# Optimization experiments

Hardware: AMD Instinct MI355X
Metric: run time of the kernel (lower is better)

The kernel has to match this reference:

```python
import jax, jax.numpy as jnp
import numpy as np

MIN_NORM = 1e-15
BALL_EPS = 4e-3  # hgcn PoincareBall eps for float32
C = 1.0          # c_in = c_out = 1


def _artanh(x):
    return jnp.arctanh(jnp.clip(x, -1.0 + 1e-7, 1.0 - 1e-7))


def _norm(x):
    return jnp.clip(jnp.linalg.norm(x, axis=-1, keepdims=True), MIN_NORM)


def proj(x, c=C):
    n = _norm(x)
    maxnorm = (1.0 - BALL_EPS) / jnp.sqrt(c)
    return jnp.where(n > maxnorm, x / n * maxnorm, x)


def expmap0(u, c=C):
    sc = jnp.sqrt(c)
    n = _norm(u)
    return jnp.tanh(sc * n) * u / (sc * n)


def logmap0(p, c=C):
    sc = jnp.sqrt(c)
    n = _norm(p)
    return _artanh(sc * n) * p / (sc * n)


def mobius_add(x, y, c=C):
    x2 = jnp.sum(x * x, -1, keepdims=True)
    y2 = jnp.sum(y * y, -1, keepdims=True)
    xy = jnp.sum(x * y, -1, keepdims=True)
    num = (1 + 2 * c * xy + c * y2) * x + (1 - c * x2) * y
    den = 1 + 2 * c * xy + c * c * x2 * y2
    return num / jnp.clip(den, MIN_NORM)


def mobius_matvec(m, x, c=C):
    # m: [out, in] torch-Linear layout; mx = x @ m.T
    sc = jnp.sqrt(c)
    xn = _norm(x)
    mx = x @ m.T
    mxn = _norm(mx)
    res = jnp.tanh(mxn / xn * _artanh(sc * xn)) * mx / (mxn * sc)
    zero = jnp.all(mx == 0, axis=-1, keepdims=True)
    return jnp.where(zero, jnp.zeros_like(res), res)


def hyp_linear(x, w, b, c=C):
    res = proj(mobius_matvec(w, x, c), c)
    hyp_bias = proj(expmap0(b[None, :], c), c)  # proj_tan0 is identity on Poincare ball
    return proj(mobius_add(res, hyp_bias, c), c)


def hyp_act(x, c_in=C, c_out=C):
    xt = jax.nn.relu(logmap0(x, c_in))
    return proj(expmap0(xt, c_out), c_out)


def mean_agg(h, src, dst, n):
    # mean of source-node features over incoming edges per destination node
    s = jax.ops.segment_sum(h[src], dst, num_segments=n)
    deg = jax.ops.segment_sum(jnp.ones((src.shape[0],), h.dtype), dst, num_segments=n)
    return s / jnp.clip(deg, 1.0)[:, None]


def setup_inputs() -> dict:
    key = jax.random.key(0)
    N, D, E = 100000, 128, 1600000  # in_features = out_features = 128
    ks = jax.random.split(key, 20)
    inp = {
        "x": jax.random.normal(ks[0], (N, D), jnp.float32) * 0.01,  # keep near ball origin
        "src_pos": jax.random.randint(ks[1], (E,), 0, N, jnp.int32),
        "dst_pos": jax.random.randint(ks[2], (E,), 0, N, jnp.int32),
        "src_neg": jax.random.randint(ks[3], (E,), 0, N, jnp.int32),
        "dst_neg": jax.random.randint(ks[4], (E,), 0, N, jnp.int32),
    }
    s = 0.01
    inp["W1b"] = jax.random.normal(ks[5], (D, 2 * D), jnp.float32) * s
    inp["b1b"] = jax.random.normal(ks[6], (D,), jnp.float32) * s
    inp["W1h"] = jax.random.normal(ks[7], (D, 2 * D), jnp.float32) * s
    inp["b1h"] = jax.random.normal(ks[8], (D,), jnp.float32) * s
    inp["W2b"] = jax.random.normal(ks[9], (2 * D, 3 * D), jnp.float32) * s
    inp["b2b"] = jax.random.normal(ks[10], (2 * D,), jnp.float32) * s
    inp["W2h"] = jax.random.normal(ks[11], (2 * D, 3 * D), jnp.float32) * s
    inp["b2h"] = jax.random.normal(ks[12], (2 * D,), jnp.float32) * s
    inp["W3b"] = jax.random.normal(ks[13], (D, 2 * D), jnp.float32) * s
    inp["b3b"] = jax.random.normal(ks[14], (D,), jnp.float32) * s
    inp["W3h"] = jax.random.normal(ks[15], (D, 2 * D), jnp.float32) * s
    inp["b3h"] = jax.random.normal(ks[16], (D,), jnp.float32) * s
    return inp


def reference(x, src_pos, dst_pos, src_neg, dst_neg,
              W1b, b1b, W1h, b1h, W2b, b2b, W2h, b2h, W3b, b3b, W3h, b3h):
    n = x.shape[0]
    # layer-1 signed neighbor means over x
    pos1 = mean_agg(x, src_pos, dst_pos, n)
    neg1 = mean_agg(x, src_neg, dst_neg, n)
    h_b1 = hyp_act(hyp_linear(jnp.concatenate([pos1, x], axis=1), W1b, b1b))
    h_n1 = hyp_act(hyp_linear(jnp.concatenate([neg1, x], axis=1), W1h, b1h))
    # layer-2 balance-theory aggregation over (h_b1, h_n1)
    pos2 = jnp.concatenate([mean_agg(h_b1, src_pos, dst_pos, n),
                            mean_agg(h_n1, src_neg, dst_neg, n)], axis=1)
    neg2 = jnp.concatenate([mean_agg(h_n1, src_pos, dst_pos, n),
                            mean_agg(h_b1, src_neg, dst_neg, n)], axis=1)
    h_b2 = hyp_act(hyp_linear(jnp.concatenate([pos2, h_b1], axis=1), W2b, b2b))
    h_n2 = hyp_act(hyp_linear(jnp.concatenate([neg2, h_n1], axis=1), W2h, b2h))
    h_b3 = hyp_act(hyp_linear(h_b2, W3b, b3b))
    h_n3 = hyp_act(hyp_linear(h_n2, W3h, b3h))
    return jnp.concatenate([h_b3, h_n3, x], axis=1)  # [N, 3*D]
```

## Files before the change

kernel.cpp:

```cpp
#include <hip/hip_runtime.h>
#include <cstdint>
#include <cstddef>

#define DEV __device__ __forceinline__

typedef unsigned int uint32;
typedef unsigned short ushort16;
typedef __bf16 bfx8 __attribute__((ext_vector_type(8)));
typedef float f32x4 __attribute__((ext_vector_type(4)));

constexpr int D = 128;
constexpr int CAP = 64;
constexpr float MINN  = 1e-15f;
constexpr float MAXN  = 1.0f - 4e-3f;
constexpr float ACLIP = 1.0f - 1e-7f;

DEV float wave_sum(float v) {
#pragma unroll
  for (int off = 32; off > 0; off >>= 1) v += __shfl_xor(v, off, 64);
  return v;
}

DEV float artanh_clip(float x) {
  x = fminf(x, ACLIP);
  return 0.5f * logf((1.0f + x) / (1.0f - x));
}

DEV uint32 f2b(float f) {
  uint32 u = __float_as_uint(f);
  u += 0x7fffu + ((u >> 16) & 1u);
  return u >> 16;
}
DEV float b2f_lo(uint32 v) { return __uint_as_float(v << 16); }
DEV float b2f_hi(uint32 v) { return __uint_as_float(v & 0xffff0000u); }

__global__ void zero_k(int* p, int n) {
  int i = blockIdx.x * 256 + threadIdx.x;
  if (i < n) p[i] = 0;
}

__global__ __launch_bounds__(256) void fillc_k(
    const int* __restrict__ sp, const int* __restrict__ dp,
    const int* __restrict__ sn, const int* __restrict__ dn, int E,
    int* __restrict__ cp, int* __restrict__ cn,
    int* __restrict__ lp, int* __restrict__ ln, int rngsz, int chunkE) {
  const int* __restrict__ src = blockIdx.y ? sn : sp;
  const int* __restrict__ dst = blockIdx.y ? dn : dp;
  int* __restrict__ cur = blockIdx.y ? cn : cp;
  int* __restrict__ lst = blockIdx.y ? ln : lp;
  const int r = blockIdx.x & 7;
  const int chunk = blockIdx.x >> 3;
  const unsigned lo = (unsigned)(r * rngsz);
  const int base = chunk * chunkE;
  const int end = min(base + chunkE, E);
  for (int i = base + (int)threadIdx.x; i < end; i += 256) {
    int d = dst[i];
    if ((unsigned)d - lo < (unsigned)rngsz) {
      int p = atomicAdd(&cur[d], 1);
      if (p < CAP) lst[(size_t)d * CAP + p] = src[i];
    }
  }
}

__global__ void rowsq_k(const float* __restrict__ x, float* __restrict__ xsq,
                        ushort16* __restrict__ xb, float* __restrict__ outx, int n) {
  int lane = threadIdx.x & 63;
  int row = blockIdx.x * 4 + (threadIdx.x >> 6);
  if (row >= n) return;
  const float2 v = *(const float2*)(x + (size_t)row * D + lane * 2);
  uint32 pk = f2b(v.x) | (f2b(v.y) << 16);
  *(uint32*)(xb + (size_t)row * D + lane * 2) = pk;
  *(float2*)(outx + (size_t)row * 384 + 256 + lane * 2) = v;
  float s = wave_sum(v.x * v.x + v.y * v.y);
  if (lane == 0) xsq[row] = s;
}

struct BiasDesc { const float* b[6]; float* hb[6]; int dim[6]; };
__global__ void bias_all_k(BiasDesc bd, float* __restrict__ hbsq) {
  int i = blockIdx.x;
  int lane = threadIdx.x;
  const float* b = bd.b[i];
  float* hb = bd.hb[i];
  int ne = bd.dim[i] / 64;
  float v[4];
  float ssq = 0.0f;
  for (int e = 0; e < ne; ++e) { v[e] = b[e * 64 + lane]; ssq += v[e] * v[e]; }
  ssq = wave_sum(ssq);
  float nr = sqrtf(ssq);
  float nc = fmaxf(nr, MINN);
  float es = tanhf(nc) / nc;
  float on = es * nr;
  float f = (on > MAXN) ? (MAXN / fmaxf(on, MINN)) : 1.0f;
  float w = es * f;
  float osq = 0.0f;
  for (int e = 0; e < ne; ++e) { v[e] *= w; osq += v[e] * v[e]; hb[e * 64 + lane] = v[e]; }
  osq = wave_sum(osq);
  if (lane == 0) hbsq[i] = osq;
}

struct WsDesc { const float* src[6]; ushort16* dst[6]; int K[6]; int total[6]; };
__global__ void wshuf_all_k(WsDesc wd) {
  int y = blockIdx.y;
  int tid = blockIdx.x * 256 + threadIdx.x;
  if (tid >= wd.total[y]) return;
  int K = wd.K[y];
  int l = tid & 63;
  int fc = tid >> 6;
  int nkc = K / 32;
  int kc = fc % nkc;
  int jt = fc / nkc;
  int col = jt * 16 + (l & 15);
  int kb = kc * 32 + (l >> 4) * 8;
  const float* src = wd.src[y] + (size_t)col * K + kb;
  uint32 o[4];
#pragma unroll
  for (int m = 0; m < 4; ++m) o[m] = f2b(src[2 * m]) | (f2b(src[2 * m + 1]) << 16);
  *(uint4*)(wd.dst[y] + (size_t)tid * 8) = make_uint4(o[0], o[1], o[2], o[3]);
}

struct AggJob {
  const ushort16* T; int lda; int ofs0; int ofs1;
  const int* cnt; const int* lst;
  ushort16* O0; ushort16* O1;
  float* S0; float* S1;
};

template <int NF>
__global__ __launch_bounds__(256) void agg2_k(AggJob ja, AggJob jbv, int n) {
  AggJob jb = blockIdx.y ? jbv : ja;
  int lane = threadIdx.x & 63;
  int row = blockIdx.x * 4 + (threadIdx.x >> 6);
  if (row >= n) return;
  int cnt = jb.cnt[row];
  int m = min(cnt, CAP);
  const int* __restrict__ lst = jb.lst + (size_t)row * CAP;
  const ushort16* __restrict__ T = jb.T;
  const int lda = jb.lda;
  const int o0 = jb.ofs0 + lane * 2;
  const int o1 = jb.ofs1 + lane * 2;
  float a0 = 0, b0 = 0, a1 = 0, b1 = 0;
  int j = 0;
  for (; j + 3 < m; j += 4) {
    size_t r0 = (size_t)lst[j] * lda, r1 = (size_t)lst[j + 1] * lda;
    size_t r2 = (size_t)lst[j + 2] * lda, r3 = (size_t)lst[j + 3] * lda;
    uint32 u0 = *(const uint32*)(T + r0 + o0);
    uint32 u1 = *(const uint32*)(T + r1 + o0);
    uint32 u2 = *(const uint32*)(T + r2 + o0);
    uint32 u3 = *(const uint32*)(T + r3 + o0);
    if (NF == 2) {
      uint32 w0 = *(const uint32*)(T + r0 + o1);
      uint32 w1 = *(const uint32*)(T + r1 + o1);
      uint32 w2 = *(const uint32*)(T + r2 + o1);
      uint32 w3 = *(const uint32*)(T + r3 + o1);
      a1 += b2f_lo(w0) + b2f_lo(w1) + b2f_lo(w2) + b2f_lo(w3);
      b1 += b2f_hi(w0) + b2f_hi(w1) + b2f_hi(w2) + b2f_hi(w3);
    }
    a0 += b2f_lo(u0) + b2f_lo(u1) + b2f_lo(u2) + b2f_lo(u3);
    b0 += b2f_hi(u0) + b2f_hi(u1) + b2f_hi(u2) + b2f_hi(u3);
  }
  for (; j < m; ++j) {
    size_t r0 = (size_t)lst[j] * lda;
    uint32 u0 = *(const uint32*)(T + r0 + o0);
    a0 += b2f_lo(u0); b0 += b2f_hi(u0);
    if (NF == 2) {
      uint32 w0 = *(const uint32*)(T + r0 + o1);
      a1 += b2f_lo(w0); b1 += b2f_hi(w0);
    }
  }
  float inv = 1.0f / fmaxf((float)cnt, 1.0f);
  a0 *= inv; b0 *= inv;
  float s = wave_sum(a0 * a0 + b0 * b0);
  *(uint32*)(jb.O0 + (size_t)row * D + lane * 2) = f2b(a0) | (f2b(b0) << 16);
  if (lane == 0) jb.S0[row] = s;
  if (NF == 2) {
    a1 *= inv; b1 *= inv;
    float s1 = wave_sum(a1 * a1 + b1 * b1);
    *(uint32*)(jb.O1 + (size_t)row * D + lane * 2) = f2b(a1) | (f2b(b1) << 16);
    if (lane == 0) jb.S1[row] = s1;
  }
}

struct GJob {
  const ushort16* p[3];
  int lda[3], ko[3];
  const ushort16* Wp;
  const float *xs0, *xs1, *xs2;
  const float *hb, *hbsq_p;
  ushort16 *ob0, *ob1; int ldob;
  float* outf; int ldof, ocol;
  float* hsq_out;
};

template <int NC, int NCT>
__global__ __launch_bounds__(256) void gemm3_k(GJob j0, GJob j1, int M) {
  GJob jb = blockIdx.y ? j1 : j0;
  __shared__ char As[16384];
  __shared__ float hbs[NCT * 64];
  __shared__ float redA[4][64][2];
  __shared__ float redB[4][64];
  __shared__ float rs[64][4];
  const int t = threadIdx.x;
  const int l = t & 63;
  const int w = t >> 6;
  const int brow = blockIdx.x * 64;
  constexpr int KC32 = NC * 4;
  const int srow = t >> 4;
  const int sco = t & 15;

  for (int c = t; c < NCT * 64; c += 256) hbs[c] = jb.hb[c];

  auto gaddr = [&](int c, int h) -> const uint4* {
    int gr = min(brow + srow + h * 16, M - 1);
    return (const uint4*)(jb.p[c] + jb.ko[c] + (size_t)gr * jb.lda[c] + sco * 8);
  };

  f32x4 acc[4][NCT] = {};
  uint4 rga[4];
#pragma unroll
  for (int h = 0; h < 4; ++h) rga[h] = *gaddr(0, h);

#pragma unroll
  for (int c = 0; c < NC; ++c) {
#pragma unroll
    for (int h = 0; h < 4; ++h) {
      int row = srow + h * 16;
      *(uint4*)(As + row * 256 + ((sco * 16) ^ ((row & 7) << 4))) = rga[h];
    }
    __syncthreads();
    if (c + 1 < NC) {
#pragma unroll
      for (int h = 0; h < 4; ++h) rga[h] = *gaddr(c + 1, h);
    }
#pragma unroll
    for (int ks = 0; ks < 4; ++ks) {
      const int kb = ks * 64 + (l >> 4) * 16;
      bfx8 a[4], b[NCT];
#pragma unroll
      for (int j = 0; j < NCT; ++j)
        b[j] = *(const bfx8*)(jb.Wp + ((size_t)((w * NCT + j) * KC32 + c * 4 + ks)) * 512 + l * 8);
#pragma unroll
      for (int i = 0; i < 4; ++i) {
        int row = i * 16 + (l & 15);
        a[i] = *(const bfx8*)(As + row * 256 + (kb ^ ((row & 7) << 4)));
      }
#pragma unroll
      for (int i = 0; i < 4; ++i)
#pragma unroll
        for (int j = 0; j < NCT; ++j)
          acc[i][j] = __builtin_amdgcn_mfma_f32_16x16x32_bf16(a[i], b[j], acc[i][j], 0, 0, 0);
    }
    __syncthreads();
  }

#pragma unroll
  for (int i = 0; i < 4; ++i)
#pragma unroll
    for (int r = 0; r < 4; ++r) {
      float s = 0.0f, xy = 0.0f;
#pragma unroll
      for (int j = 0; j < NCT; ++j) {
        float m = acc[i][j][r];
        int col = w * (NCT * 16) + j * 16 + (l & 15);
        s += m * m;
        xy += m * hbs[col];
      }
#pragma unroll
      for (int off = 1; off < 16; off <<= 1) {
        s += __shfl_xor(s, off, 64);
        xy += __shfl_xor(xy, off, 64);
      }
      if ((l & 15) == 0) {
        int row = i * 16 + (l >> 4) * 4 + r;
        redA[w][row][0] = s;
        redA[w][row][1] = xy;
      }
    }
  __syncthreads();

  if (t < 64 && brow + t < M) {
    float ssq = redA[0][t][0] + redA[1][t][0] + redA[2][t][0] + redA[3][t][0];
    float xyr = redA[0][t][1] + redA[1][t][1] + redA[2][t][1] + redA[3][t][1];
    float mxn_raw = sqrtf(ssq);
    float xnsq = jb.xs0[brow + t];
    if (jb.xs1) xnsq += jb.xs1[brow + t];
    if (jb.xs2) xnsq += jb.xs2[brow + t];
    float xn = fmaxf(sqrtf(xnsq), MINN);
    float mxn = fmaxf(mxn_raw, MINN);
    float scal = tanhf(mxn / xn * artanh_clip(xn)) / mxn;
    float rn_raw = scal * mxn_raw;
    if (rn_raw > MAXN) { scal *= MAXN / fmaxf(rn_raw, MINN); rn_raw = MAXN; }
    float xyv = scal * xyr;
    float x2 = rn_raw * rn_raw;
    float y2 = *jb.hbsq_p;
    float den = fmaxf(1.0f + 2.0f * xyv + x2 * y2, MINN);
    float ax = (1.0f + 2.0f * xyv + y2) / den;
    float ay = (1.0f - x2) / den;
    float vsq = scal * scal * ssq;
    float psq = fmaxf(ax * ax * vsq + 2.0f * ax * ay * xyv + ay * ay * y2, 0.0f);
    float pn_raw = sqrtf(psq);
    float f2s = (pn_raw > MAXN) ? (MAXN / fmaxf(pn_raw, MINN)) : 1.0f;
    pn_raw = fminf(pn_raw, MAXN);
    float pn = fmaxf(pn_raw, MINN);
    float la = artanh_clip(pn) / pn * f2s;
    rs[t][0] = scal * ax;
    rs[t][1] = ay;
    rs[t][2] = la;
  }
  __syncthreads();

#pragma unroll
  for (int i = 0; i < 4; ++i)
#pragma unroll
    for (int r = 0; r < 4; ++r) {
      int row = i * 16 + (l >> 4) * 4 + r;
      float c1 = rs[row][0], c2 = rs[row][1];
      float pp = 0.0f;
#pragma unroll
      for (int j = 0; j < NCT; ++j) {
        int col = w * (NCT * 16) + j * 16 + (l & 15);
        float p = c1 * acc[i][j][r] + c2 * hbs[col];
        p = fmaxf(p, 0.0f);
        acc[i][j][r] = p;
        pp += p * p;
      }
#pragma unroll
      for (int off = 1; off < 16; off <<= 1) pp += __shfl_xor(pp, off, 64);
      if ((l & 15) == 0) redB[w][row] = pp;
    }
  __syncthreads();

  if (t < 64 && brow + t < M) {
    float ppos = redB[0][t] + redB[1][t] + redB[2][t] + redB[3][t];
    float la = rs[t][2];
    float tsq = la * la * ppos;
    float tn_raw = sqrtf(tsq);
    float tnc = fmaxf(tn_raw, MINN);
    float es = tanhf(tnc) / tnc;
    float on_raw = es * tn_raw;
    float f3 = (on_raw > MAXN) ? (MAXN / fmaxf(on_raw, MINN)) : 1.0f;
    float wsc = es * f3;
    float g = wsc * la;
    rs[t][3] = g;
    if (jb.hsq_out) jb.hsq_out[brow + t] = g * g * ppos;
  }
  __syncthreads();

#pragma unroll
  for (int i = 0; i < 4; ++i)
#pragma unroll
    for (int r = 0; r < 4; ++r) {
      int row = i * 16 + (l >> 4) * 4 + r;
      int gr = brow + row;
      if (gr < M) {
        float g = rs[row][3];
#pragma unroll
        for (int j = 0; j < NCT; ++j) {
          int col = w * (NCT * 16) + j * 16 + (l & 15);
          float o = g * acc[i][j][r];
          if (jb.ob0) {
            ushort16* ob = (col < 128) ? jb.ob0 : jb.ob1;
            ob[(size_t)gr * jb.ldob + (col & 127)] = (ushort16)f2b(o);
          } else {
            jb.outf[(size_t)gr * jb.ldof + jb.ocol + col] = o;
          }
        }
      }
    }
}

extern "C" void kernel_launch(void* const* d_in, const int* in_sizes, int n_in,
                              void* d_out, int out_size, void* d_ws, size_t ws_size,
                              hipStream_t stream) {
  const float* x = (const float*)d_in[0];
  const int* src_pos = (const int*)d_in[1];
  const int* dst_pos = (const int*)d_in[2];
  const int* src_neg = (const int*)d_in[3];
  const int* dst_neg = (const int*)d_in[4];
  const float* W1b = (const float*)d_in[5];
  const float* b1b = (const float*)d_in[6];
  const float* W1h = (const float*)d_in[7];
  const float* b1h = (const float*)d_in[8];
  const float* W2b = (const float*)d_in[9];
  const float* b2b = (const float*)d_in[10];
  const float* W2h = (const float*)d_in[11];
  const float* b2h = (const float*)d_in[12];
  const float* W3b = (const float*)d_in[13];
  const float* b3b = (const float*)d_in[14];
  const float* W3h = (const float*)d_in[15];
  const float* b3h = (const float*)d_in[16];

  const int N = in_sizes[0] / D;
  const int E = in_sizes[1];

  int* iw = (int*)d_ws;
  size_t io = 0;
  int* cur_p = iw + io;  io += N;
  int* cur_n = iw + io;  io += N;
  int* lst_p = iw + io;  io += (size_t)N * CAP;
  int* lst_n = iw + io;  io += (size_t)N * CAP;
  io = (io + 63) & ~(size_t)63;

  float* fw = (float*)(iw + io);
  size_t fo = 0;
  float* xsq = fw + fo;    fo += N;
  float* hsq_b1 = fw + fo; fo += N;
  float* hsq_n1 = fw + fo; fo += N;
  float* hsq_b2 = fw + fo; fo += N;
  float* hsq_n2 = fw + fo; fo += N;
  float* ssq_p1 = fw + fo; fo += N;
  float* ssq_n1 = fw + fo; fo += N;
  float* ssq_pp = fw + fo; fo += N;
  float* ssq_np = fw + fo; fo += N;
  float* ssq_nn = fw + fo; fo += N;
  float* ssq_bn = fw + fo; fo += N;
  float* hbase = fw + fo;  fo += 1056;
  fo = (fo + 31) & ~(size_t)31;

  ushort16* SB = (ushort16*)(fw + fo);
  const size_t NSB = (size_t)N * D;
  ushort16* TA = SB;
  ushort16* H1 = SB + NSB;
  ushort16* TD = SB + 3 * NSB;
  ushort16* TE = SB + 4 * NSB;
  ushort16* TF = SB + 5 * NSB;
  ushort16* wb1b = SB + 6 * NSB;
  ushort16* wb1h = wb1b + 32768;
  ushort16* wb2b = wb1h + 32768;
  ushort16* wb2h = wb2b + 98304;
  ushort16* wb3b = wb2h + 98304;
  ushort16* wb3h = wb3b + 32768;

  float* outf = (float*)d_out;

  float* hb1b = hbase + 0;
  float* hb1h = hbase + 128;
  float* hb2b = hbase + 256;
  float* hb2h = hbase + 512;
  float* hb3b = hbase + 768;
  float* hb3h = hbase + 896;
  float* hbsq = hbase + 1024;

  const int grow = (N + 3) / 4;
  const int gf = (N + 63) / 64;
  const int rngsz = (N + 7) / 8;
  const int chunkE = (E + 255) / 256;
  const int gpart = 256 * 8;

  zero_k<<<(2 * N + 255) / 256, 256, 0, stream>>>(cur_p, 2 * N);
  fillc_k<<<dim3(gpart, 2), 256, 0, stream>>>(src_pos, dst_pos, src_neg, dst_neg, E,
                                              cur_p, cur_n, lst_p, lst_n, rngsz, chunkE);

  rowsq_k<<<grow, 256, 0, stream>>>(x, xsq, TA, outf, N);
  {
    BiasDesc bd;
    bd.b[0] = b1b; bd.hb[0] = hb1b; bd.dim[0] = 128;
    bd.b[1] = b1h; bd.hb[1] = hb1h; bd.dim[1] = 128;
    bd.b[2] = b2b; bd.hb[2] = hb2b; bd.dim[2] = 256;
    bd.b[3] = b2h; bd.hb[3] = hb2h; bd.dim[3] = 256;
    bd.b[4] = b3b; bd.hb[4] = hb3b; bd.dim[4] = 128;
    bd.b[5] = b3h; bd.hb[5] = hb3h; bd.dim[5] = 128;
    bias_all_k<<<6, 64, 0, stream>>>(bd, hbsq);
  }
  {
    WsDesc wd;
    wd.src[0] = W1b; wd.dst[0] = wb1b; wd.K[0] = 256; wd.total[0] = 8 * 8 * 64;
    wd.src[1] = W1h; wd.dst[1] = wb1h; wd.K[1] = 256; wd.total[1] = 8 * 8 * 64;
    wd.src[2] = W2b; wd.dst[2] = wb2b; wd.K[2] = 384; wd.total[2] = 16 * 12 * 64;
    wd.src[3] = W2h; wd.dst[3] = wb2h; wd.K[3] = 384; wd.total[3] = 16 * 12 * 64;
    wd.src[4] = W3b; wd.dst[4] = wb3b; wd.K[4] = 256; wd.total[4] = 8 * 8 * 64;
    wd.src[5] = W3h; wd.dst[5] = wb3h; wd.K[5] = 256; wd.total[5] = 8 * 8 * 64;
    wshuf_all_k<<<dim3(48, 6), 256, 0, stream>>>(wd);
  }

  {
    AggJob jp{TA, 128, 0, 0, cur_p, lst_p, TD, nullptr, ssq_p1, nullptr};
    AggJob jn{TA, 128, 0, 0, cur_n, lst_n, TE, nullptr, ssq_n1, nullptr};
    agg2_k<1><<<dim3(grow, 2), 256, 0, stream>>>(jp, jn, N);
  }
  {
    GJob ja{}, jh{};
    ja.p[0] = TD; ja.lda[0] = 128; ja.ko[0] = 0;
    ja.p[1] = TA; ja.lda[1] = 128; ja.ko[1] = 0;
    ja.Wp = wb1b; ja.xs0 = ssq_p1; ja.xs1 = xsq; ja.xs2 = nullptr;
    ja.hb = hb1b; ja.hbsq_p = hbsq + 0;
    ja.ob0 = H1; ja.ob1 = nullptr; ja.ldob = 256;
    ja.outf = nullptr; ja.ldof = 0; ja.ocol = 0; ja.hsq_out = hsq_b1;
    jh = ja;
    jh.p[0] = TE; jh.Wp = wb1h; jh.xs0 = ssq_n1;
    jh.hb = hb1h; jh.hbsq_p = hbsq + 1; jh.ob0 = H1 + 128; jh.hsq_out = hsq_n1;
    gemm3_k<2, 2><<<dim3(gf, 2), 256, 0, stream>>>(ja, jh, N);
  }

  {
    AggJob jp{H1, 256, 0, 128, cur_p, lst_p, TD, TE, ssq_pp, ssq_np};
    AggJob jn{H1, 256, 128, 0, cur_n, lst_n, TA, TF, ssq_nn, ssq_bn};
    agg2_k<2><<<dim3(grow, 2), 256, 0, stream>>>(jp, jn, N);
  }
  {
    GJob ja{}, jh{};
    ja.p[0] = TD; ja.lda[0] = 128; ja.ko[0] = 0;
    ja.p[1] = TA; ja.lda[1] = 128; ja.ko[1] = 0;
    ja.p[2] = H1; ja.lda[2] = 256; ja.ko[2] = 0;
    ja.Wp = wb2b; ja.xs0 = ssq_pp; ja.xs1 = ssq_nn; ja.xs2 = hsq_b1;
    ja.hb = hb2b; ja.hbsq_p = hbsq + 2;
    ja.ob0 = TD; ja.ob1 = TA; ja.ldob = 128;
    ja.outf = nullptr; ja.ldof = 0; ja.ocol = 0; ja.hsq_out = hsq_b2;
    jh = ja;
    jh.p[0] = TE; jh.p[1] = TF; jh.ko[2] = 128;
    jh.Wp = wb2h; jh.xs0 = ssq_np; jh.xs1 = ssq_bn; jh.xs2 = hsq_n1;
    jh.hb = hb2h; jh.hbsq_p = hbsq + 3;
    jh.ob0 = TE; jh.ob1 = TF; jh.hsq_out = hsq_n2;
    gemm3_k<3, 4><<<dim3(gf, 2), 256, 0, stream>>>(ja, jh, N);
  }

  {
    GJob ja{}, jh{};
    ja.p[0] = TD; ja.lda[0] = 128; ja.ko[0] = 0;
    ja.p[1] = TA; ja.lda[1] = 128; ja.ko[1] = 0;
    ja.Wp = wb3b; ja.xs0 = hsq_b2; ja.xs1 = nullptr; ja.xs2 = nullptr;
    ja.hb = hb3b; ja.hbsq_p = hbsq + 4;
    ja.ob0 = nullptr; ja.ob1 = nullptr; ja.ldob = 0;
    ja.outf = outf; ja.ldof = 3 * D; ja.ocol = 0; ja.hsq_out = nullptr;
    jh = ja;
    jh.p[0] = TE; jh.p[1] = TF;
    jh.Wp = wb3h; jh.xs0 = hsq_n2;
    jh.hb = hb3h; jh.hbsq_p = hbsq + 5; jh.ocol = 128;
    gemm3_k<2, 2><<<dim3(gf, 2), 256, 0, stream>>>(ja, jh, N);
  }
}
```

Measured before the change: 859.5 us.

## Widen gather loads in neighbor aggregation and fold counter zeroing into rowsq

The aggregation kernel now gathers 8-byte chunks per lane, covering the full 256-col H1 row in a single pass for layer 2. For layer 1, half-waves process alternate neighbors and are combined with a shuffle. Loads are batched 16 at a time for more memory-level parallelism, and the output pointers for the negative job are swapped to match the contiguous row layout. The separate zero kernel is merged into rowsq_k to remove one launch. This adds register pressure from the 16-wide unroll.

```diff
diff --git a/kernel.cpp b/kernel.cpp
--- a/kernel.cpp
+++ b/kernel.cpp
@@ -33,11 +33,6 @@
 }
 DEV float b2f_lo(uint32 v) { return __uint_as_float(v << 16); }
 DEV float b2f_hi(uint32 v) { return __uint_as_float(v & 0xffff0000u); }
-
-__global__ void zero_k(int* p, int n) {
-  int i = blockIdx.x * 256 + threadIdx.x;
-  if (i < n) p[i] = 0;
-}
 
 __global__ __launch_bounds__(256) void fillc_k(
     const int* __restrict__ sp, const int* __restrict__ dp,
@@ -63,7 +58,10 @@
 }
 
 __global__ void rowsq_k(const float* __restrict__ x, float* __restrict__ xsq,
-                        ushort16* __restrict__ xb, float* __restrict__ outx, int n) {
+                        ushort16* __restrict__ xb, float* __restrict__ outx,
+                        int* __restrict__ curz, int nz, int n) {
+  int gid = blockIdx.x * 256 + (int)threadIdx.x;
+  if (gid < nz) curz[gid] = 0;
   int lane = threadIdx.x & 63;
   int row = blockIdx.x * 4 + (threadIdx.x >> 6);
   if (row >= n) return;
@@ -119,64 +117,98 @@
 }
 
 struct AggJob {
-  const ushort16* T; int lda; int ofs0; int ofs1;
+  const char* T;
   const int* cnt; const int* lst;
-  ushort16* O0; ushort16* O1;
-  float* S0; float* S1;
+  ushort16* OutLo; ushort16* OutHi;
+  float* Slo; float* Shi;
 };
 
 template <int NF>
 __global__ __launch_bounds__(256) void agg2_k(AggJob ja, AggJob jbv, int n) {
   AggJob jb = blockIdx.y ? jbv : ja;
-  int lane = threadIdx.x & 63;
-  int row = blockIdx.x * 4 + (threadIdx.x >> 6);
+  const int l = threadIdx.x & 63;
+  const int row = blockIdx.x * 4 + ((int)threadIdx.x >> 6);
   if (row >= n) return;
-  int cnt = jb.cnt[row];
-  int m = min(cnt, CAP);
+  const int cnt = jb.cnt[row];
+  const int m = min(cnt, CAP);
   const int* __restrict__ lst = jb.lst + (size_t)row * CAP;
-  const ushort16* __restrict__ T = jb.T;
-  const int lda = jb.lda;
-  const int o0 = jb.ofs0 + lane * 2;
-  const int o1 = jb.ofs1 + lane * 2;
-  float a0 = 0, b0 = 0, a1 = 0, b1 = 0;
+  const char* __restrict__ T = jb.T;
+  float a0 = 0, a1 = 0, a2 = 0, a3 = 0;
   int j = 0;
-  for (; j + 3 < m; j += 4) {
-    size_t r0 = (size_t)lst[j] * lda, r1 = (size_t)lst[j + 1] * lda;
-    size_t r2 = (size_t)lst[j + 2] * lda, r3 = (size_t)lst[j + 3] * lda;
-    uint32 u0 = *(const uint32*)(T + r0 + o0);
-    uint32 u1 = *(const uint32*)(T + r1 + o0);
-    uint32 u2 = *(const uint32*)(T + r2 + o0);
-    uint32 u3 = *(const uint32*)(T + r3 + o0);
-    if (NF == 2) {
-      uint32 w0 = *(const uint32*)(T + r0 + o1);
-      uint32 w1 = *(const uint32*)(T + r1 + o1);
-      uint32 w2 = *(const uint32*)(T + r2 + o1);
-      uint32 w3 = *(const uint32*)(T + r3 + o1);
-      a1 += b2f_lo(w0) + b2f_lo(w1) + b2f_lo(w2) + b2f_lo(w3);
-      b1 += b2f_hi(w0) + b2f_hi(w1) + b2f_hi(w2) + b2f_hi(w3);
-    }
-    a0 += b2f_lo(u0) + b2f_lo(u1) + b2f_lo(u2) + b2f_lo(u3);
-    b0 += b2f_hi(u0) + b2f_hi(u1) + b2f_hi(u2) + b2f_hi(u3);
-  }
-  for (; j < m; ++j) {
-    size_t r0 = (size_t)lst[j] * lda;
-    uint32 u0 = *(const uint32*)(T + r0 + o0);
-    a0 += b2f_lo(u0); b0 += b2f_hi(u0);
-    if (NF == 2) {
-      uint32 w0 = *(const uint32*)(T + r0 + o1);
-      a1 += b2f_lo(w0); b1 += b2f_hi(w0);
-    }
+  if (NF == 2) {
+    const int off = l * 8;
+    for (; j + 15 < m; j += 16) {
+      uint2 v[16];
+#pragma unroll
+      for (int q = 0; q < 16; ++q)
+        v[q] = *(const uint2*)(T + (size_t)lst[j + q] * 512 + off);
+#pragma unroll
+      for (int q = 0; q < 16; ++q) {
+        a0 += b2f_lo(v[q].x); a1 += b2f_hi(v[q].x);
+        a2 += b2f_lo(v[q].y); a3 += b2f_hi(v[q].y);
+      }
+    }
+    for (; j + 3 < m; j += 4) {
+      uint2 v[4];
+#pragma unroll
+      for (int q = 0; q < 4; ++q)
+        v[q] = *(const uint2*)(T + (size_t)lst[j + q] * 512 + off);
+#pragma unroll
+      for (int q = 0; q < 4; ++q) {
+        a0 += b2f_lo(v[q].x); a1 += b2f_hi(v[q].x);
+        a2 += b2f_lo(v[q].y); a3 += b2f_hi(v[q].y);
+      }
+    }
+    for (; j < m; ++j) {
+      uint2 v = *(const uint2*)(T + (size_t)lst[j] * 512 + off);
+      a0 += b2f_lo(v.x); a1 += b2f_hi(v.x);
+      a2 += b2f_lo(v.y); a3 += b2f_hi(v.y);
+    }
+  } else {
+    const int off = (l & 31) * 8;
+    const int g = l >> 5;
+    for (; j + 15 < m; j += 16) {
+      uint2 v[8];
+#pragma unroll
+      for (int q = 0; q < 8; ++q)
+        v[q] = *(const uint2*)(T + (size_t)lst[j + g + 2 * q] * 256 + off);
+#pragma unroll
+      for (int q = 0; q < 8; ++q) {
+        a0 += b2f_lo(v[q].x); a1 += b2f_hi(v[q].x);
+        a2 += b2f_lo(v[q].y); a3 += b2f_hi(v[q].y);
+      }
+    }
+    for (; j + 1 < m; j += 2) {
+      uint2 v = *(const uint2*)(T + (size_t)lst[j + g] * 256 + off);
+      a0 += b2f_lo(v.x); a1 += b2f_hi(v.x);
+      a2 += b2f_lo(v.y); a3 += b2f_hi(v.y);
+    }
+    if (j < m && g == 0) {
+      uint2 v = *(const uint2*)(T + (size_t)lst[j] * 256 + off);
+      a0 += b2f_lo(v.x); a1 += b2f_hi(v.x);
+      a2 += b2f_lo(v.y); a3 += b2f_hi(v.y);
+    }
+    a0 += __shfl_xor(a0, 32, 64);
+    a1 += __shfl_xor(a1, 32, 64);
+    a2 += __shfl_xor(a2, 32, 64);
+    a3 += __shfl_xor(a3, 32, 64);
   }
   float inv = 1.0f / fmaxf((float)cnt, 1.0f);
-  a0 *= inv; b0 *= inv;
-  float s = wave_sum(a0 * a0 + b0 * b0);
-  *(uint32*)(jb.O0 + (size_t)row * D + lane * 2) = f2b(a0) | (f2b(b0) << 16);
-  if (lane == 0) jb.S0[row] = s;
+  a0 *= inv; a1 *= inv; a2 *= inv; a3 *= inv;
+  float sq = a0 * a0 + a1 * a1 + a2 * a2 + a3 * a3;
+#pragma unroll
+  for (int o2 = 1; o2 < 32; o2 <<= 1) sq += __shfl_xor(sq, o2, 64);
+  uint2 o;
+  o.x = f2b(a0) | (f2b(a1) << 16);
+  o.y = f2b(a2) | (f2b(a3) << 16);
   if (NF == 2) {
-    a1 *= inv; b1 *= inv;
-    float s1 = wave_sum(a1 * a1 + b1 * b1);
-    *(uint32*)(jb.O1 + (size_t)row * D + lane * 2) = f2b(a1) | (f2b(b1) << 16);
-    if (lane == 0) jb.S1[row] = s1;
+    ushort16* Out = (l < 32) ? jb.OutLo : jb.OutHi;
+    *(uint2*)((char*)Out + (size_t)row * 256 + (l & 31) * 8) = o;
+    if (l == 0) jb.Slo[row] = sq;
+    if (l == 32) jb.Shi[row] = sq;
+  } else {
+    if (l < 32) *(uint2*)((char*)jb.OutLo + (size_t)row * 256 + l * 8) = o;
+    if (l == 0) jb.Slo[row] = sq;
   }
 }
 
@@ -446,11 +478,9 @@
   const int chunkE = (E + 255) / 256;
   const int gpart = 256 * 8;
 
-  zero_k<<<(2 * N + 255) / 256, 256, 0, stream>>>(cur_p, 2 * N);
+  rowsq_k<<<grow, 256, 0, stream>>>(x, xsq, TA, outf, cur_p, 2 * N, N);
   fillc_k<<<dim3(gpart, 2), 256, 0, stream>>>(src_pos, dst_pos, src_neg, dst_neg, E,
                                               cur_p, cur_n, lst_p, lst_n, rngsz, chunkE);
-
-  rowsq_k<<<grow, 256, 0, stream>>>(x, xsq, TA, outf, N);
   {
     BiasDesc bd;
     bd.b[0] = b1b; bd.hb[0] = hb1b; bd.dim[0] = 128;
@@ -473,8 +503,8 @@
   }
 
   {
-    AggJob jp{TA, 128, 0, 0, cur_p, lst_p, TD, nullptr, ssq_p1, nullptr};
-    AggJob jn{TA, 128, 0, 0, cur_n, lst_n, TE, nullptr, ssq_n1, nullptr};
+    AggJob jp{(const char*)TA, cur_p, lst_p, TD, nullptr, ssq_p1, nullptr};
+    AggJob jn{(const char*)TA, cur_n, lst_n, TE, nullptr, ssq_n1, nullptr};
     agg2_k<1><<<dim3(grow, 2), 256, 0, stream>>>(jp, jn, N);
   }
   {
@@ -492,8 +522,8 @@
   }
 
   {
-    AggJob jp{H1, 256, 0, 128, cur_p, lst_p, TD, TE, ssq_pp, ssq_np};
-    AggJob jn{H1, 256, 128, 0, cur_n, lst_n, TA, TF, ssq_nn, ssq_bn};
+    AggJob jp{(const char*)H1, cur_p, lst_p, TD, TE, ssq_pp, ssq_np};
+    AggJob jn{(const char*)H1, cur_n, lst_n, TF, TA, ssq_bn, ssq_nn};
     agg2_k<2><<<dim3(grow, 2), 256, 0, stream>>>(jp, jn, N);
   }
   {
```

New measurement: 866.4 us, median of 2. About the same (+0.8%).
